# Optimization experiments

Measured on AMD Instinct MI355X. Metric: run time of the kernel, lower is better.

## Reference

```python
import math
import jax, jax.numpy as jnp
import numpy as np

D_MODEL = 1024
NUM_HEADS = 16
HEAD_DIM = D_MODEL // NUM_HEADS
B, T = 2, 2048


def setup_inputs() -> dict:
    key = jax.random.key(0)
    ks = jax.random.split(key, 11)
    s = 0.02
    inp = {
        'x':  jax.random.normal(ks[0], (B, T, D_MODEL), dtype=jnp.float32),
        'Wq': jax.random.normal(ks[1], (D_MODEL, D_MODEL), dtype=jnp.float32) * s,
        'bq': jax.random.normal(ks[2], (D_MODEL,), dtype=jnp.float32) * s,
        'Wk': jax.random.normal(ks[3], (D_MODEL, D_MODEL), dtype=jnp.float32) * s,
        'bk': jax.random.normal(ks[4], (D_MODEL,), dtype=jnp.float32) * s,
        'Wv': jax.random.normal(ks[5], (D_MODEL, D_MODEL), dtype=jnp.float32) * s,
        'bv': jax.random.normal(ks[6], (D_MODEL,), dtype=jnp.float32) * s,
        'Wt': jax.random.normal(ks[7], (D_MODEL, D_MODEL), dtype=jnp.float32) * s,
        'bt': jax.random.normal(ks[8], (D_MODEL,), dtype=jnp.float32) * s,
        'Wo': jax.random.normal(ks[9], (D_MODEL, D_MODEL), dtype=jnp.float32) * s,
        'bo': jax.random.normal(ks[10], (D_MODEL,), dtype=jnp.float32) * s,
    }
    return inp


def reference(x, Wq, bq, Wk, bk, Wv, bv, Wt, bt, Wo, bo):
    Bx, Tx, D = x.shape
    H, hd = NUM_HEADS, HEAD_DIM
    scale = 1.0 / math.sqrt(hd)

    def proj(W, b):
        # (B,T,D) -> (B,H,T,hd); torch Linear uses x @ W.T + b
        return (x @ W.T + b).reshape(Bx, Tx, H, hd).transpose(0, 2, 1, 3)

    q = proj(Wq, bq)
    k = proj(Wk, bk)
    v = proj(Wv, bv)
    t = proj(Wt, bt)

    # dot-product term: (B,H,T,T)
    scores = jnp.einsum('bhqd,bhkd->bhqk', q, k)
    # triplet term: cumsum over key positions of (k*v)/sqrt(hd)
    kv_cumsum = jnp.cumsum(k * v * scale, axis=2)  # (B,H,T,hd)
    scores = scores + jnp.einsum('bhqd,bhkd->bhqk', q * t, kv_cumsum)
    scores = scores * scale

    # causal mask: position j > i forbidden
    causal = jnp.tril(jnp.ones((Tx, Tx), dtype=bool))
    scores = jnp.where(causal[None, None], scores, jnp.float32(-jnp.inf))

    attn = jax.nn.softmax(scores, axis=-1)  # stable max-subtract internally
    out = jnp.einsum('bhqk,bhkd->bhqd', attn, v)
    out = out.transpose(0, 2, 1, 3).reshape(Bx, Tx, D)
    return out @ Wo.T + bo
```

## Files before the change

kernel.cpp:

```cpp
#include <hip/hip_runtime.h>
#include <hip/hip_bf16.h>

typedef unsigned short u16;
typedef __attribute__((ext_vector_type(8))) short bf16x8;
typedef __attribute__((ext_vector_type(4))) float f32x4;
typedef __attribute__((ext_vector_type(4))) unsigned int u32x4;

#define LOG2E 1.44269504088896340736f

static __device__ __forceinline__ float b2f(u16 u) {
    union { float f; unsigned int i; } v; v.i = ((unsigned int)u) << 16; return v.f;
}
static __device__ __forceinline__ u16 f2b(float f) {
    unsigned int x = __builtin_bit_cast(unsigned int, f);
    unsigned int r = (x + 0x7fffu + ((x >> 16) & 1u)) >> 16;
    return (u16)r;
}
static __device__ __forceinline__ void gll16(const u16* g, u16* l) {
    __builtin_amdgcn_global_load_lds((const __attribute__((address_space(1))) void*)g,
                                     (__attribute__((address_space(3))) void*)l, 16, 0, 0);
}
static __device__ __forceinline__ float fexp2(float x) {
    float r; asm("v_exp_f32 %0, %1" : "=v"(r) : "v"(x)); return r;
}

__global__ __launch_bounds__(256) void cvt_all(const float* __restrict__ x,
                                               const float* __restrict__ w0, const float* __restrict__ w1,
                                               const float* __restrict__ w2, const float* __restrict__ w3,
                                               const float* __restrict__ w4, u16* __restrict__ dst) {
    size_t c = (size_t)blockIdx.x * 256 + threadIdx.x;
    size_t e = c * 4;
    const float* s; size_t off;
    const size_t M4 = (size_t)4 << 20, M1 = (size_t)1 << 20;
    if (e < M4) { s = x; off = e; }
    else {
        size_t r = e - M4; int wsel = (int)(r >> 20); off = r & (M1 - 1);
        s = wsel == 0 ? w0 : wsel == 1 ? w1 : wsel == 2 ? w2 : wsel == 3 ? w3 : w4;
    }
    float4 v = *(const float4*)(s + off);
    u16* d = dst + e;
    d[0] = f2b(v.x); d[1] = f2b(v.y); d[2] = f2b(v.z); d[3] = f2b(v.w);
}

template<int WM>
static __device__ __forceinline__ void gemm_body(const u16* __restrict__ A, const u16* __restrict__ W,
                                                 const float* __restrict__ bias, void* __restrict__ outp,
                                                 int mode, u16* Al, u16* Bl, int tm, int tn) {
    const int tid = threadIdx.x, lane = tid & 63, w = tid >> 6;
    const int wr = w >> 1, wc = w & 1;
    const int l15 = lane & 15, lhi = lane >> 4;

    f32x4 acc[WM][4] = {};

    for (int kt = 0; kt < 16; ++kt) {
        const int k0 = kt * 64;
        #pragma unroll
        for (int i = 0; i < WM; ++i) {
            int rl = i * 32 + w * 8 + (lane >> 3);
            int c  = (lane & 7) ^ (rl & 7);
            gll16(A + (size_t)(tm + rl) * 1024 + k0 + c * 8, Al + (i * 32 + w * 8) * 64);
        }
        #pragma unroll
        for (int i = 0; i < 4; ++i) {
            int rl = i * 32 + w * 8 + (lane >> 3);
            int c  = (lane & 7) ^ (rl & 7);
            gll16(W + (size_t)(tn + rl) * 1024 + k0 + c * 8, Bl + (i * 32 + w * 8) * 64);
        }
        __syncthreads();
        #pragma unroll
        for (int ks = 0; ks < 2; ++ks) {
            bf16x8 af[WM], bfr[4];
            #pragma unroll
            for (int mi = 0; mi < WM; ++mi) {
                int row = wr * (WM * 16) + mi * 16 + l15;
                int cc = (ks * 4 + lhi) ^ (row & 7);
                af[mi] = *(const bf16x8*)(Al + row * 64 + cc * 8);
            }
            #pragma unroll
            for (int ni = 0; ni < 4; ++ni) {
                int row = wc * 64 + ni * 16 + l15;
                int cc = (ks * 4 + lhi) ^ (row & 7);
                bfr[ni] = *(const bf16x8*)(Bl + row * 64 + cc * 8);
            }
            #pragma unroll
            for (int mi = 0; mi < WM; ++mi)
                #pragma unroll
                for (int ni = 0; ni < 4; ++ni)
                    acc[mi][ni] = __builtin_amdgcn_mfma_f32_16x16x32_bf16(af[mi], bfr[ni], acc[mi][ni], 0, 0, 0);
        }
        __syncthreads();
    }

    float bcol[4];
    #pragma unroll
    for (int ni = 0; ni < 4; ++ni) bcol[ni] = bias[tn + wc * 64 + ni * 16 + l15];

    #pragma unroll
    for (int mi = 0; mi < WM; ++mi)
        #pragma unroll
        for (int ni = 0; ni < 4; ++ni)
            #pragma unroll
            for (int r = 0; r < 4; ++r) {
                int rg = tm + wr * (WM * 16) + mi * 16 + lhi * 4 + r;
                int cg = tn + wc * 64 + ni * 16 + l15;
                float v = acc[mi][ni][r] + bcol[ni];
                if (mode == 2) {
                    ((float*)outp)[(size_t)rg * 1024 + cg] = v;
                } else {
                    int b = rg >> 11, t = rg & 2047, h = cg >> 6, d = cg & 63;
                    if (mode == 0)
                        ((u16*)outp)[(((size_t)(b * 16 + h)) * 2048 + t) * 128 + d] = f2b(v);
                    else
                        ((u16*)outp)[(((size_t)(b * 16 + h)) * 2048 + t) * 64 + d] = f2b(v);
                }
            }
}

struct ProjArgs {
    const u16* W[4];
    const float* b[4];
    u16* out[4];
};

__global__ __launch_bounds__(256) void gemm_proj(const u16* __restrict__ A, ProjArgs pa) {
    __shared__ u16 Al[128 * 64];
    __shared__ u16 Bl[128 * 64];
    const int d = blockIdx.x + 8 * blockIdx.y + 256 * blockIdx.z;
    const int c = d & 7, wtn = d >> 3;
    const int z = c >> 1, yh = c & 1;
    const int yy = yh * 16 + (wtn >> 3);
    const int xx = wtn & 7;
    gemm_body<4>(A, pa.W[z], pa.b[z], pa.out[z], (z < 2) ? 0 : 1, Al, Bl, yy * 128, xx * 128);
}


__global__ __launch_bounds__(256) void gemm_out2(const u16* __restrict__ A, const u16* __restrict__ W,
                                                 const float* __restrict__ bias, void* __restrict__ out) {
    __shared__ u16 Al[64 * 64];
    __shared__ u16 Bl[128 * 64];
    const int d = blockIdx.x + 8 * blockIdx.y;
    const int c = d & 7, wtn = d >> 3;
    const int yy = c * 8 + (wtn >> 3);
    const int xx = wtn & 7;
    gemm_body<2>(A, W, bias, out, 2, Al, Bl, yy * 64, xx * 128);
}

__global__ __launch_bounds__(256) void fuse_small(u16* __restrict__ Qa, const u16* __restrict__ Tp,
                                                  const u16* __restrict__ V, u16* __restrict__ VT,
                                                  u16* __restrict__ Ka) {
    __shared__ char shmem[64 * 72 * 2];
    const int b = blockIdx.x, tid = threadIdx.x;

    if (b < 2048) {
        int idx = b * 256 + tid;
        int tg = idx >> 3, dc = idx & 7;
        bf16x8 q = *(const bf16x8*)(Qa + (size_t)tg * 128 + dc * 8);
        bf16x8 tt = *(const bf16x8*)(Tp + (size_t)tg * 64 + dc * 8);
        bf16x8 o;
        #pragma unroll
        for (int j = 0; j < 8; ++j) o[j] = (short)f2b(b2f((u16)q[j]) * b2f((u16)tt[j]));
        *(bf16x8*)(Qa + (size_t)tg * 128 + 64 + dc * 8) = o;
    } else if (b < 3072) {
        u16 (*tile)[72] = (u16(*)[72])shmem;
        const int r0 = b - 2048;
        const int bh = r0 >> 5, tc = r0 & 31;
        const u16* Vh = V + ((size_t)bh * 2048 + tc * 64) * 64;
        u16* VTh = VT + (size_t)bh * 64 * 2048 + tc * 64;
        for (int i = 0; i < 2; ++i) {
            int f = i * 256 + tid;
            int r = f >> 3, dc = f & 7;
            bf16x8 v = *(const bf16x8*)(Vh + r * 64 + dc * 8);
            #pragma unroll
            for (int j = 0; j < 8; ++j) tile[dc * 8 + j][r] = (u16)v[j];
        }
        __syncthreads();
        for (int i = 0; i < 2; ++i) {
            int f = i * 256 + tid;
            int d = f >> 3, t8 = (f & 7) * 8;
            bf16x8 o;
            #pragma unroll
            for (int j = 0; j < 8; ++j) {
                int pos = t8 + j;
                int key = (pos & 32) + 16 * ((pos >> 2) & 1) + 4 * ((pos >> 3) & 3) + (pos & 3);
                o[j] = (short)tile[d][key];
            }
            *(bf16x8*)(VTh + (size_t)d * 2048 + t8) = o;
        }
    } else {
        float4* sums = (float4*)shmem;
        const int r0 = b - 3072;
        const int bh = r0 & 31, dg = r0 >> 5;
        u16* Kh = Ka + (size_t)bh * 2048 * 128;
        const u16* Vh = V + (size_t)bh * 2048 * 64;
        const int quad = tid & 3, c = tid >> 2;
        const int d0 = dg * 16 + quad * 4;
        float s0 = 0.f, s1 = 0.f, s2 = 0.f, s3 = 0.f;
        for (int i = 0; i < 32; ++i) {
            int t = c * 32 + i;
            ushort4 kv = *(const ushort4*)(Kh + (size_t)t * 128 + d0);
            ushort4 vv = *(const ushort4*)(Vh + (size_t)t * 64 + d0);
            s0 += b2f(kv.x) * b2f(vv.x);
            s1 += b2f(kv.y) * b2f(vv.y);
            s2 += b2f(kv.z) * b2f(vv.z);
            s3 += b2f(kv.w) * b2f(vv.w);
        }
        float4 sv; sv.x = s0; sv.y = s1; sv.z = s2; sv.w = s3;
        sums[c * 4 + quad] = sv;
        __syncthreads();
        float4 run; run.x = run.y = run.z = run.w = 0.f;
        for (int cc = 0; cc < c; ++cc) {
            float4 ss = sums[cc * 4 + quad];
            run.x += ss.x; run.y += ss.y; run.z += ss.z; run.w += ss.w;
        }
        for (int i = 0; i < 32; ++i) {
            int t = c * 32 + i;
            ushort4 kv = *(const ushort4*)(Kh + (size_t)t * 128 + d0);
            ushort4 vv = *(const ushort4*)(Vh + (size_t)t * 64 + d0);
            run.x += b2f(kv.x) * b2f(vv.x);
            run.y += b2f(kv.y) * b2f(vv.y);
            run.z += b2f(kv.z) * b2f(vv.z);
            run.w += b2f(kv.w) * b2f(vv.w);
            ushort4 o;
            o.x = f2b(run.x * 0.125f); o.y = f2b(run.y * 0.125f);
            o.z = f2b(run.z * 0.125f); o.w = f2b(run.w * 0.125f);
            *(ushort4*)(Kh + (size_t)t * 128 + 64 + d0) = o;
        }
    }
}

__global__ __launch_bounds__(256, 3) void attn5(const u16* __restrict__ Qa, const u16* __restrict__ Ka,
                                                const u16* __restrict__ VT, u16* __restrict__ Obuf) {
    const int wg = blockIdx.x;
    const int xcd = wg & 7, slot = wg >> 3;
    const int bh = xcd * 4 + (slot >> 4);
    const int qp = slot & 15;
    const int tiL = qp, tiH = 31 - qp;
    const int q0L = tiL * 64, q0H = tiH * 64;
    const int NT = tiH + 1;
    const u16* Qh = Qa + (size_t)bh * 2048 * 128;
    const u16* Kh = Ka + (size_t)bh * 2048 * 128;
    const u16* VTh = VT + (size_t)bh * 64 * 2048;

    __shared__ u16 Kl[2][64 * 128];
    __shared__ u16 Vl[2][64 * 64];

    const int tid = threadIdx.x, lane = tid & 63, w = tid >> 6;
    const int l15 = lane & 15, lhi = lane >> 4;
    const float SC = 0.125f * LOG2E;

    bf16x8 qfL[4], qfH[4];
    #pragma unroll
    for (int ks = 0; ks < 4; ++ks) {
        bf16x8 a = *(const bf16x8*)(Qh + (size_t)(q0L + w * 16 + l15) * 128 + ks * 32 + lhi * 8);
        bf16x8 b = *(const bf16x8*)(Qh + (size_t)(q0H + w * 16 + l15) * 128 + ks * 32 + lhi * 8);
        bf16x8 oa, ob;
        #pragma unroll
        for (int j = 0; j < 8; ++j) {
            oa[j] = (short)f2b(b2f((u16)a[j]) * SC);
            ob[j] = (short)f2b(b2f((u16)b[j]) * SC);
        }
        qfL[ks] = oa; qfH[ks] = ob;
    }

    f32x4 accL[4] = {}, accH[4] = {};
    float lsL = 0.f, lsH = 0.f;

    auto STAGE = [&](int buf, int ti) {
        const int kv0 = ti * 64;
        #pragma unroll
        for (int i = 0; i < 4; ++i) {
            int lr = i * 16 + w * 4 + lhi;
            int c = l15 ^ (lr & 15);
            gll16(Kh + (size_t)(kv0 + lr) * 128 + c * 8, &Kl[buf][(i * 16 + w * 4) * 128]);
        }
        #pragma unroll
        for (int i = 0; i < 2; ++i) {
            int dr = i * 32 + w * 8 + (lane >> 3);
            int c = (lane & 7) ^ (dr & 7);
            gll16(VTh + (size_t)dr * 2048 + kv0 + c * 8, &Vl[buf][(i * 32 + w * 8) * 64]);
        }
    };

    STAGE(0, 0);
    asm volatile("s_waitcnt vmcnt(0)" ::: "memory");
    __builtin_amdgcn_s_barrier();

    for (int ti = 0; ti < NT; ++ti) {
        const int cur = ti & 1;
        if (ti + 1 < NT) STAGE(cur ^ 1, ti + 1);
        const bool doL = (ti <= tiL);

        f32x4 sH[4] = {}, sL[4] = {};
        #pragma unroll
        for (int ks = 0; ks < 4; ++ks) {
            bf16x8 kf[4];
            #pragma unroll
            for (int k2 = 0; k2 < 4; ++k2) {
                int kl = k2 * 16 + l15;
                int cc = (ks * 4 + lhi) ^ l15;
                kf[k2] = *(const bf16x8*)(&Kl[cur][kl * 128 + cc * 8]);
            }
            __builtin_amdgcn_s_setprio(1);
            #pragma unroll
            for (int k2 = 0; k2 < 4; ++k2)
                sH[k2] = __builtin_amdgcn_mfma_f32_16x16x32_bf16(kf[k2], qfH[ks], sH[k2], 0, 0, 0);
            if (doL) {
                #pragma unroll
                for (int k2 = 0; k2 < 4; ++k2)
                    sL[k2] = __builtin_amdgcn_mfma_f32_16x16x32_bf16(kf[k2], qfL[ks], sL[k2], 0, 0, 0);
            }
            __builtin_amdgcn_s_setprio(0);
        }

        auto FINISH = [&](f32x4* sacc, f32x4* acc, float& lsum, bool diag) {
            float p[4][4];
            #pragma unroll
            for (int k2 = 0; k2 < 4; ++k2)
                #pragma unroll
                for (int r = 0; r < 4; ++r) {
                    float s = sacc[k2][r];
                    if (diag) {
                        int key = k2 * 16 + lhi * 4 + r;
                        int qq = w * 16 + l15;
                        s = (key <= qq) ? s : -1e30f;
                    }
                    float pe = fexp2(s);
                    p[k2][r] = pe;
                    lsum += pe;
                }
            bf16x8 pf[2];
            #pragma unroll
            for (int ks2 = 0; ks2 < 2; ++ks2) {
                unsigned int w0, w1, w2, w3;
                asm("v_cvt_pk_bf16_f32 %0, %1, %2" : "=v"(w0) : "v"(p[2 * ks2][0]),     "v"(p[2 * ks2][1]));
                asm("v_cvt_pk_bf16_f32 %0, %1, %2" : "=v"(w1) : "v"(p[2 * ks2][2]),     "v"(p[2 * ks2][3]));
                asm("v_cvt_pk_bf16_f32 %0, %1, %2" : "=v"(w2) : "v"(p[2 * ks2 + 1][0]), "v"(p[2 * ks2 + 1][1]));
                asm("v_cvt_pk_bf16_f32 %0, %1, %2" : "=v"(w3) : "v"(p[2 * ks2 + 1][2]), "v"(p[2 * ks2 + 1][3]));
                u32x4 t = {w0, w1, w2, w3};
                pf[ks2] = __builtin_bit_cast(bf16x8, t);
            }
            #pragma unroll
            for (int ks2 = 0; ks2 < 2; ++ks2) {
                __builtin_amdgcn_s_setprio(1);
                #pragma unroll
                for (int dt = 0; dt < 4; ++dt) {
                    int dd = dt * 16 + l15;
                    int cc = (ks2 * 4 + lhi) ^ (dd & 7);
                    bf16x8 vf = *(const bf16x8*)(&Vl[cur][dd * 64 + cc * 8]);
                    acc[dt] = __builtin_amdgcn_mfma_f32_16x16x32_bf16(pf[ks2], vf, acc[dt], 0, 0, 0);
                }
                __builtin_amdgcn_s_setprio(0);
            }
        };

        FINISH(sH, accH, lsH, ti == tiH);
        if (doL) FINISH(sL, accL, lsL, ti == tiL);

        asm volatile("s_waitcnt vmcnt(0)" ::: "memory");
        __builtin_amdgcn_s_barrier();
    }

    lsH += __shfl_xor(lsH, 16, 64); lsH += __shfl_xor(lsH, 32, 64);
    lsL += __shfl_xor(lsL, 16, 64); lsL += __shfl_xor(lsL, 32, 64);
    float invH[4], invL[4];
    #pragma unroll
    for (int r = 0; r < 4; ++r) {
        invH[r] = 1.0f / __shfl(lsH, lhi * 4 + r, 64);
        invL[r] = 1.0f / __shfl(lsL, lhi * 4 + r, 64);
    }
    #pragma unroll
    for (int dt = 0; dt < 4; ++dt)
        #pragma unroll
        for (int r = 0; r < 4; ++r) {
            int cr = lhi * 4 + r;
            int dd = dt * 16 + l15;
            int qgL = q0L + w * 16 + cr;
            int qgH = q0H + w * 16 + cr;
            size_t nL = (size_t)(bh >> 4) * 2048 + qgL;
            size_t nH = (size_t)(bh >> 4) * 2048 + qgH;
            Obuf[nL * 1024 + (bh & 15) * 64 + dd] = f2b(accL[dt][r] * invL[r]);
            Obuf[nH * 1024 + (bh & 15) * 64 + dd] = f2b(accH[dt][r] * invH[r]);
        }
}

extern "C" void kernel_launch(void* const* d_in, const int* in_sizes, int n_in,
                              void* d_out, int out_size, void* d_ws, size_t ws_size,
                              hipStream_t stream) {
    (void)in_sizes; (void)n_in; (void)out_size; (void)ws_size;
    const float* x  = (const float*)d_in[0];
    const float* Wq = (const float*)d_in[1];
    const float* bq = (const float*)d_in[2];
    const float* Wk = (const float*)d_in[3];
    const float* bk = (const float*)d_in[4];
    const float* Wv = (const float*)d_in[5];
    const float* bv = (const float*)d_in[6];
    const float* Wt = (const float*)d_in[7];
    const float* bt = (const float*)d_in[8];
    const float* Wo = (const float*)d_in[9];
    const float* bo = (const float*)d_in[10];

    const size_t M1 = 1024u * 1024u;
    u16* xb   = (u16*)d_ws;
    u16* wq   = xb + 4 * M1;
    u16* wk   = wq + M1;
    u16* wv   = wk + M1;
    u16* wt   = wv + M1;
    u16* wo   = wt + M1;
    u16* Qa   = wo + M1;
    u16* Kaa  = Qa + 8 * M1;
    u16* Vtm  = Kaa + 8 * M1;
    u16* Ttm  = Vtm + 4 * M1;
    u16* Obuf = Ttm + 4 * M1;
    u16* VTg  = xb;

    cvt_all<<<9216, 256, 0, stream>>>(x, Wq, Wk, Wv, Wt, Wo, xb);

    ProjArgs pa;
    pa.W[0] = wq; pa.W[1] = wk; pa.W[2] = wv; pa.W[3] = wt;
    pa.b[0] = bq; pa.b[1] = bk; pa.b[2] = bv; pa.b[3] = bt;
    pa.out[0] = Qa; pa.out[1] = Kaa; pa.out[2] = Vtm; pa.out[3] = Ttm;
    gemm_proj<<<dim3(8, 32, 4), 256, 0, stream>>>(xb, pa);

    fuse_small<<<3200, 256, 0, stream>>>(Qa, Ttm, Vtm, VTg, Kaa);

    attn5<<<512, 256, 0, stream>>>(Qa, Kaa, VTg, Obuf);

    gemm_out2<<<dim3(8, 64), 256, 0, stream>>>(Obuf, wo, bo, d_out);
}
```

Measured before the change: 138.6 us.

## Triple-buffer K/V tiles and software-pipeline QK of next tile with softmax-PV

The attention kernel moves from double to triple buffering of K and V tiles in LDS, with separate staging so that K is prefetched three tiles ahead and V two tiles ahead. The loop is software-pipelined: the QK^T MFMAs for tile ti+1 are issued before the exp/PV work for tile ti, so matrix and vector work can overlap. Partial vmcnt waits replace the full drain. In exchange, LDS use rises to three buffers and launch bounds drop from 3 to 2 blocks per CU, and holding two sets of score accumulators adds register pressure.

Result: no change. 140.2 us (+1.1%).

```diff
diff --git a/kernel.cpp b/kernel.cpp
--- a/kernel.cpp
+++ b/kernel.cpp
@@ -132,7 +132,6 @@
     const int xx = wtn & 7;
     gemm_body<4>(A, pa.W[z], pa.b[z], pa.out[z], (z < 2) ? 0 : 1, Al, Bl, yy * 128, xx * 128);
 }
-
 
 __global__ __launch_bounds__(256) void gemm_out2(const u16* __restrict__ A, const u16* __restrict__ W,
                                                  const float* __restrict__ bias, void* __restrict__ out) {
@@ -228,7 +227,7 @@
     }
 }
 
-__global__ __launch_bounds__(256, 3) void attn5(const u16* __restrict__ Qa, const u16* __restrict__ Ka,
+__global__ __launch_bounds__(256, 2) void attn8(const u16* __restrict__ Qa, const u16* __restrict__ Ka,
                                                 const u16* __restrict__ VT, u16* __restrict__ Obuf) {
     const int wg = blockIdx.x;
     const int xcd = wg & 7, slot = wg >> 3;
@@ -241,8 +240,8 @@
     const u16* Kh = Ka + (size_t)bh * 2048 * 128;
     const u16* VTh = VT + (size_t)bh * 64 * 2048;
 
-    __shared__ u16 Kl[2][64 * 128];
-    __shared__ u16 Vl[2][64 * 64];
+    __shared__ u16 Kl[3][64 * 128];
+    __shared__ u16 Vl[3][64 * 64];
 
     const int tid = threadIdx.x, lane = tid & 63, w = tid >> 6;
     const int l15 = lane & 15, lhi = lane >> 4;
@@ -265,32 +264,27 @@
     f32x4 accL[4] = {}, accH[4] = {};
     float lsL = 0.f, lsH = 0.f;
 
-    auto STAGE = [&](int buf, int ti) {
-        const int kv0 = ti * 64;
+    auto STAGE_V = [&](int ti) {
+        const int kv0 = ti * 64, buf = ti % 3;
+        #pragma unroll
+        for (int i = 0; i < 2; ++i) {
+            int dr = i * 32 + w * 8 + (lane >> 3);
+            int c = (lane & 7) ^ (dr & 7);
+            gll16(VTh + (size_t)dr * 2048 + kv0 + c * 8, &Vl[buf][(i * 32 + w * 8) * 64]);
+        }
+    };
+    auto STAGE_K = [&](int ti) {
+        const int kv0 = ti * 64, buf = ti % 3;
         #pragma unroll
         for (int i = 0; i < 4; ++i) {
             int lr = i * 16 + w * 4 + lhi;
             int c = l15 ^ (lr & 15);
             gll16(Kh + (size_t)(kv0 + lr) * 128 + c * 8, &Kl[buf][(i * 16 + w * 4) * 128]);
         }
-        #pragma unroll
-        for (int i = 0; i < 2; ++i) {
-            int dr = i * 32 + w * 8 + (lane >> 3);
-            int c = (lane & 7) ^ (dr & 7);
-            gll16(VTh + (size_t)dr * 2048 + kv0 + c * 8, &Vl[buf][(i * 32 + w * 8) * 64]);
-        }
     };
 
-    STAGE(0, 0);
-    asm volatile("s_waitcnt vmcnt(0)" ::: "memory");
-    __builtin_amdgcn_s_barrier();
-
-    for (int ti = 0; ti < NT; ++ti) {
-        const int cur = ti & 1;
-        if (ti + 1 < NT) STAGE(cur ^ 1, ti + 1);
-        const bool doL = (ti <= tiL);
-
-        f32x4 sH[4] = {}, sL[4] = {};
+    auto QK = [&](int ti, bool doL, f32x4* sH, f32x4* sL) {
+        const int cur = ti % 3;
         #pragma unroll
         for (int ks = 0; ks < 4; ++ks) {
             bf16x8 kf[4];
@@ -311,53 +305,77 @@
             }
             __builtin_amdgcn_s_setprio(0);
         }
-
-        auto FINISH = [&](f32x4* sacc, f32x4* acc, float& lsum, bool diag) {
-            float p[4][4];
-            #pragma unroll
-            for (int k2 = 0; k2 < 4; ++k2)
-                #pragma unroll
-                for (int r = 0; r < 4; ++r) {
-                    float s = sacc[k2][r];
-                    if (diag) {
-                        int key = k2 * 16 + lhi * 4 + r;
-                        int qq = w * 16 + l15;
-                        s = (key <= qq) ? s : -1e30f;
-                    }
-                    float pe = fexp2(s);
-                    p[k2][r] = pe;
-                    lsum += pe;
+    };
+
+    auto FINISH = [&](int ti, f32x4* sacc, f32x4* acc, float& lsum, bool diag) {
+        const int cur = ti % 3;
+        float p[4][4];
+        #pragma unroll
+        for (int k2 = 0; k2 < 4; ++k2)
+            #pragma unroll
+            for (int r = 0; r < 4; ++r) {
+                float s = sacc[k2][r];
+                if (diag) {
+                    int key = k2 * 16 + lhi * 4 + r;
+                    int qq = w * 16 + l15;
+                    s = (key <= qq) ? s : -1e30f;
                 }
-            bf16x8 pf[2];
-            #pragma unroll
-            for (int ks2 = 0; ks2 < 2; ++ks2) {
-                unsigned int w0, w1, w2, w3;
-                asm("v_cvt_pk_bf16_f32 %0, %1, %2" : "=v"(w0) : "v"(p[2 * ks2][0]),     "v"(p[2 * ks2][1]));
-                asm("v_cvt_pk_bf16_f32 %0, %1, %2" : "=v"(w1) : "v"(p[2 * ks2][2]),     "v"(p[2 * ks2][3]));
-                asm("v_cvt_pk_bf16_f32 %0, %1, %2" : "=v"(w2) : "v"(p[2 * ks2 + 1][0]), "v"(p[2 * ks2 + 1][1]));
-                asm("v_cvt_pk_bf16_f32 %0, %1, %2" : "=v"(w3) : "v"(p[2 * ks2 + 1][2]), "v"(p[2 * ks2 + 1][3]));
-                u32x4 t = {w0, w1, w2, w3};
-                pf[ks2] = __builtin_bit_cast(bf16x8, t);
-            }
-            #pragma unroll
-            for (int ks2 = 0; ks2 < 2; ++ks2) {
-                __builtin_amdgcn_s_setprio(1);
-                #pragma unroll
-                for (int dt = 0; dt < 4; ++dt) {
-                    int dd = dt * 16 + l15;
-                    int cc = (ks2 * 4 + lhi) ^ (dd & 7);
-                    bf16x8 vf = *(const bf16x8*)(&Vl[cur][dd * 64 + cc * 8]);
-                    acc[dt] = __builtin_amdgcn_mfma_f32_16x16x32_bf16(pf[ks2], vf, acc[dt], 0, 0, 0);
-                }
-                __builtin_amdgcn_s_setprio(0);
-            }
-        };
-
-        FINISH(sH, accH, lsH, ti == tiH);
-        if (doL) FINISH(sL, accL, lsL, ti == tiL);
-
-        asm volatile("s_waitcnt vmcnt(0)" ::: "memory");
-        __builtin_amdgcn_s_barrier();
+                float pe = fexp2(s);
+                p[k2][r] = pe;
+                lsum += pe;
+            }
+        bf16x8 pf[2];
+        #pragma unroll
+        for (int ks2 = 0; ks2 < 2; ++ks2) {
+            unsigned int w0, w1, w2, w3;
+            asm("v_cvt_pk_bf16_f32 %0, %1, %2" : "=v"(w0) : "v"(p[2 * ks2][0]),     "v"(p[2 * ks2][1]));
+            asm("v_cvt_pk_bf16_f32 %0, %1, %2" : "=v"(w1) : "v"(p[2 * ks2][2]),     "v"(p[2 * ks2][3]));
+            asm("v_cvt_pk_bf16_f32 %0, %1, %2" : "=v"(w2) : "v"(p[2 * ks2 + 1][0]), "v"(p[2 * ks2 + 1][1]));
+            asm("v_cvt_pk_bf16_f32 %0, %1, %2" : "=v"(w3) : "v"(p[2 * ks2 + 1][2]), "v"(p[2 * ks2 + 1][3]));
+            u32x4 t = {w0, w1, w2, w3};
+            pf[ks2] = __builtin_bit_cast(bf16x8, t);
+        }
+        #pragma unroll
+        for (int ks2 = 0; ks2 < 2; ++ks2) {
+            __builtin_amdgcn_s_setprio(1);
+            #pragma unroll
+            for (int dt = 0; dt < 4; ++dt) {
+                int dd = dt * 16 + l15;
+                int cc = (ks2 * 4 + lhi) ^ (dd & 7);
+                bf16x8 vf = *(const bf16x8*)(&Vl[cur][dd * 64 + cc * 8]);
+                acc[dt] = __builtin_amdgcn_mfma_f32_16x16x32_bf16(pf[ks2], vf, acc[dt], 0, 0, 0);
+            }
+            __builtin_amdgcn_s_setprio(0);
+        }
+    };
+
+    STAGE_V(0); STAGE_V(1);
+    STAGE_K(0); STAGE_K(1); STAGE_K(2);
+    asm volatile("s_waitcnt vmcnt(0)" ::: "memory");
+    __builtin_amdgcn_s_barrier();
+
+    f32x4 sHc[4] = {}, sLc[4] = {};
+    QK(0, true, sHc, sLc);
+
+    for (int ti = 0; ti < NT; ++ti) {
+        if (ti + 2 < NT) STAGE_V(ti + 2);
+        if (ti + 3 < NT) STAGE_K(ti + 3);
+
+        f32x4 sHn[4] = {}, sLn[4] = {};
+        const bool doLn = (ti + 1 <= tiL);
+        if (ti + 1 < NT) QK(ti + 1, doLn, sHn, sLn);
+
+        FINISH(ti, sHc, accH, lsH, ti == tiH);
+        if (ti <= tiL) FINISH(ti, sLc, accL, lsL, ti == tiL);
+
+        #pragma unroll
+        for (int k2 = 0; k2 < 4; ++k2) { sHc[k2] = sHn[k2]; sLc[k2] = sLn[k2]; }
+
+        if (ti + 1 < NT) {
+            if (ti + 3 < NT) asm volatile("s_waitcnt vmcnt(4)" ::: "memory");
+            else             asm volatile("s_waitcnt vmcnt(0)" ::: "memory");
+            __builtin_amdgcn_s_barrier();
+        }
     }
 
     lsH += __shfl_xor(lsH, 16, 64); lsH += __shfl_xor(lsH, 32, 64);
@@ -423,7 +441,7 @@
 
     fuse_small<<<3200, 256, 0, stream>>>(Qa, Ttm, Vtm, VTg, Kaa);
 
-    attn5<<<512, 256, 0, stream>>>(Qa, Kaa, VTg, Obuf);
+    attn8<<<512, 256, 0, stream>>>(Qa, Kaa, VTg, Obuf);
 
     gemm_out2<<<dim3(8, 64), 256, 0, stream>>>(Obuf, wo, bo, d_out);
 }
```

## Split paired-query attention blocks into one query tile per workgroup

Applied to the files above, without the earlier changes.

The attention kernel no longer pairs a low and a high query tile in one workgroup to balance causal work. It now launches 1024 workgroups, each handling a single 64-row query tile, with the longest tiles scheduled first. This halves register use per workgroup and drops the occupancy hint, aiming for more resident waves and simpler code. The cost is that K/V tiles are no longer shared between two query tiles, so staging traffic per unit of compute rises, and load balance now depends on the descending-order schedule.

Result: no change. 140.9 us (+1.6%).

```diff
diff --git a/kernel.cpp b/kernel.cpp
--- a/kernel.cpp
+++ b/kernel.cpp
@@ -132,7 +132,6 @@
     const int xx = wtn & 7;
     gemm_body<4>(A, pa.W[z], pa.b[z], pa.out[z], (z < 2) ? 0 : 1, Al, Bl, yy * 128, xx * 128);
 }
-
 
 __global__ __launch_bounds__(256) void gemm_out2(const u16* __restrict__ A, const u16* __restrict__ W,
                                                  const float* __restrict__ bias, void* __restrict__ out) {
@@ -228,15 +227,14 @@
     }
 }
 
-__global__ __launch_bounds__(256, 3) void attn5(const u16* __restrict__ Qa, const u16* __restrict__ Ka,
-                                                const u16* __restrict__ VT, u16* __restrict__ Obuf) {
+__global__ __launch_bounds__(256) void attn9(const u16* __restrict__ Qa, const u16* __restrict__ Ka,
+                                             const u16* __restrict__ VT, u16* __restrict__ Obuf) {
     const int wg = blockIdx.x;
     const int xcd = wg & 7, slot = wg >> 3;
-    const int bh = xcd * 4 + (slot >> 4);
-    const int qp = slot & 15;
-    const int tiL = qp, tiH = 31 - qp;
-    const int q0L = tiL * 64, q0H = tiH * 64;
-    const int NT = tiH + 1;
+    const int bh = xcd * 4 + (slot >> 5);
+    const int qb = 31 - (slot & 31);
+    const int q0 = qb * 64;
+    const int NT = qb + 1;
     const u16* Qh = Qa + (size_t)bh * 2048 * 128;
     const u16* Kh = Ka + (size_t)bh * 2048 * 128;
     const u16* VTh = VT + (size_t)bh * 64 * 2048;
@@ -248,22 +246,18 @@
     const int l15 = lane & 15, lhi = lane >> 4;
     const float SC = 0.125f * LOG2E;
 
-    bf16x8 qfL[4], qfH[4];
+    bf16x8 qf[4];
     #pragma unroll
     for (int ks = 0; ks < 4; ++ks) {
-        bf16x8 a = *(const bf16x8*)(Qh + (size_t)(q0L + w * 16 + l15) * 128 + ks * 32 + lhi * 8);
-        bf16x8 b = *(const bf16x8*)(Qh + (size_t)(q0H + w * 16 + l15) * 128 + ks * 32 + lhi * 8);
-        bf16x8 oa, ob;
-        #pragma unroll
-        for (int j = 0; j < 8; ++j) {
-            oa[j] = (short)f2b(b2f((u16)a[j]) * SC);
-            ob[j] = (short)f2b(b2f((u16)b[j]) * SC);
-        }
-        qfL[ks] = oa; qfH[ks] = ob;
+        bf16x8 a = *(const bf16x8*)(Qh + (size_t)(q0 + w * 16 + l15) * 128 + ks * 32 + lhi * 8);
+        bf16x8 oa;
+        #pragma unroll
+        for (int j = 0; j < 8; ++j) oa[j] = (short)f2b(b2f((u16)a[j]) * SC);
+        qf[ks] = oa;
     }
 
-    f32x4 accL[4] = {}, accH[4] = {};
-    float lsL = 0.f, lsH = 0.f;
+    f32x4 acc[4] = {};
+    float lsum = 0.f;
 
     auto STAGE = [&](int buf, int ti) {
         const int kv0 = ti * 64;
@@ -288,9 +282,8 @@
     for (int ti = 0; ti < NT; ++ti) {
         const int cur = ti & 1;
         if (ti + 1 < NT) STAGE(cur ^ 1, ti + 1);
-        const bool doL = (ti <= tiL);
-
-        f32x4 sH[4] = {}, sL[4] = {};
+
+        f32x4 s4[4] = {};
         #pragma unroll
         for (int ks = 0; ks < 4; ++ks) {
             bf16x8 kf[4];
@@ -303,83 +296,67 @@
             __builtin_amdgcn_s_setprio(1);
             #pragma unroll
             for (int k2 = 0; k2 < 4; ++k2)
-                sH[k2] = __builtin_amdgcn_mfma_f32_16x16x32_bf16(kf[k2], qfH[ks], sH[k2], 0, 0, 0);
-            if (doL) {
-                #pragma unroll
-                for (int k2 = 0; k2 < 4; ++k2)
-                    sL[k2] = __builtin_amdgcn_mfma_f32_16x16x32_bf16(kf[k2], qfL[ks], sL[k2], 0, 0, 0);
-            }
+                s4[k2] = __builtin_amdgcn_mfma_f32_16x16x32_bf16(kf[k2], qf[ks], s4[k2], 0, 0, 0);
             __builtin_amdgcn_s_setprio(0);
         }
 
-        auto FINISH = [&](f32x4* sacc, f32x4* acc, float& lsum, bool diag) {
-            float p[4][4];
-            #pragma unroll
-            for (int k2 = 0; k2 < 4; ++k2)
-                #pragma unroll
-                for (int r = 0; r < 4; ++r) {
-                    float s = sacc[k2][r];
-                    if (diag) {
-                        int key = k2 * 16 + lhi * 4 + r;
-                        int qq = w * 16 + l15;
-                        s = (key <= qq) ? s : -1e30f;
-                    }
-                    float pe = fexp2(s);
-                    p[k2][r] = pe;
-                    lsum += pe;
+        const bool diag = (ti == NT - 1);
+        float p[4][4];
+        #pragma unroll
+        for (int k2 = 0; k2 < 4; ++k2)
+            #pragma unroll
+            for (int r = 0; r < 4; ++r) {
+                float s = s4[k2][r];
+                if (diag) {
+                    int key = k2 * 16 + lhi * 4 + r;
+                    int qq = w * 16 + l15;
+                    s = (key <= qq) ? s : -1e30f;
                 }
-            bf16x8 pf[2];
-            #pragma unroll
-            for (int ks2 = 0; ks2 < 2; ++ks2) {
-                unsigned int w0, w1, w2, w3;
-                asm("v_cvt_pk_bf16_f32 %0, %1, %2" : "=v"(w0) : "v"(p[2 * ks2][0]),     "v"(p[2 * ks2][1]));
-                asm("v_cvt_pk_bf16_f32 %0, %1, %2" : "=v"(w1) : "v"(p[2 * ks2][2]),     "v"(p[2 * ks2][3]));
-                asm("v_cvt_pk_bf16_f32 %0, %1, %2" : "=v"(w2) : "v"(p[2 * ks2 + 1][0]), "v"(p[2 * ks2 + 1][1]));
-                asm("v_cvt_pk_bf16_f32 %0, %1, %2" : "=v"(w3) : "v"(p[2 * ks2 + 1][2]), "v"(p[2 * ks2 + 1][3]));
-                u32x4 t = {w0, w1, w2, w3};
-                pf[ks2] = __builtin_bit_cast(bf16x8, t);
-            }
-            #pragma unroll
-            for (int ks2 = 0; ks2 < 2; ++ks2) {
-                __builtin_amdgcn_s_setprio(1);
-                #pragma unroll
-                for (int dt = 0; dt < 4; ++dt) {
-                    int dd = dt * 16 + l15;
-                    int cc = (ks2 * 4 + lhi) ^ (dd & 7);
-                    bf16x8 vf = *(const bf16x8*)(&Vl[cur][dd * 64 + cc * 8]);
-                    acc[dt] = __builtin_amdgcn_mfma_f32_16x16x32_bf16(pf[ks2], vf, acc[dt], 0, 0, 0);
-                }
-                __builtin_amdgcn_s_setprio(0);
-            }
-        };
-
-        FINISH(sH, accH, lsH, ti == tiH);
-        if (doL) FINISH(sL, accL, lsL, ti == tiL);
+                float pe = fexp2(s);
+                p[k2][r] = pe;
+                lsum += pe;
+            }
+        bf16x8 pf[2];
+        #pragma unroll
+        for (int ks2 = 0; ks2 < 2; ++ks2) {
+            unsigned int w0, w1, w2, w3;
+            asm("v_cvt_pk_bf16_f32 %0, %1, %2" : "=v"(w0) : "v"(p[2 * ks2][0]),     "v"(p[2 * ks2][1]));
+            asm("v_cvt_pk_bf16_f32 %0, %1, %2" : "=v"(w1) : "v"(p[2 * ks2][2]),     "v"(p[2 * ks2][3]));
+            asm("v_cvt_pk_bf16_f32 %0, %1, %2" : "=v"(w2) : "v"(p[2 * ks2 + 1][0]), "v"(p[2 * ks2 + 1][1]));
+            asm("v_cvt_pk_bf16_f32 %0, %1, %2" : "=v"(w3) : "v"(p[2 * ks2 + 1][2]), "v"(p[2 * ks2 + 1][3]));
+            u32x4 t = {w0, w1, w2, w3};
+            pf[ks2] = __builtin_bit_cast(bf16x8, t);
+        }
+        #pragma unroll
+        for (int ks2 = 0; ks2 < 2; ++ks2) {
+            __builtin_amdgcn_s_setprio(1);
+            #pragma unroll
+            for (int dt = 0; dt < 4; ++dt) {
+                int dd = dt * 16 + l15;
+                int cc = (ks2 * 4 + lhi) ^ (dd & 7);
+                bf16x8 vf = *(const bf16x8*)(&Vl[cur][dd * 64 + cc * 8]);
+                acc[dt] = __builtin_amdgcn_mfma_f32_16x16x32_bf16(pf[ks2], vf, acc[dt], 0, 0, 0);
+            }
+            __builtin_amdgcn_s_setprio(0);
+        }
 
         asm volatile("s_waitcnt vmcnt(0)" ::: "memory");
         __builtin_amdgcn_s_barrier();
     }
 
-    lsH += __shfl_xor(lsH, 16, 64); lsH += __shfl_xor(lsH, 32, 64);
-    lsL += __shfl_xor(lsL, 16, 64); lsL += __shfl_xor(lsL, 32, 64);
-    float invH[4], invL[4];
+    lsum += __shfl_xor(lsum, 16, 64); lsum += __shfl_xor(lsum, 32, 64);
+    float inv[4];
     #pragma unroll
-    for (int r = 0; r < 4; ++r) {
-        invH[r] = 1.0f / __shfl(lsH, lhi * 4 + r, 64);
-        invL[r] = 1.0f / __shfl(lsL, lhi * 4 + r, 64);
-    }
+    for (int r = 0; r < 4; ++r) inv[r] = 1.0f / __shfl(lsum, lhi * 4 + r, 64);
     #pragma unroll
     for (int dt = 0; dt < 4; ++dt)
         #pragma unroll
         for (int r = 0; r < 4; ++r) {
             int cr = lhi * 4 + r;
             int dd = dt * 16 + l15;
-            int qgL = q0L + w * 16 + cr;
-            int qgH = q0H + w * 16 + cr;
-            size_t nL = (size_t)(bh >> 4) * 2048 + qgL;
-            size_t nH = (size_t)(bh >> 4) * 2048 + qgH;
-            Obuf[nL * 1024 + (bh & 15) * 64 + dd] = f2b(accL[dt][r] * invL[r]);
-            Obuf[nH * 1024 + (bh & 15) * 64 + dd] = f2b(accH[dt][r] * invH[r]);
+            int qg = q0 + w * 16 + cr;
+            size_t n = (size_t)(bh >> 4) * 2048 + qg;
+            Obuf[n * 1024 + (bh & 15) * 64 + dd] = f2b(acc[dt][r] * inv[r]);
         }
 }
 
@@ -423,7 +400,7 @@
 
     fuse_small<<<3200, 256, 0, stream>>>(Qa, Ttm, Vtm, VTg, Kaa);
 
-    attn5<<<512, 256, 0, stream>>>(Qa, Kaa, VTg, Obuf);
+    attn9<<<1024, 256, 0, stream>>>(Qa, Kaa, VTg, Obuf);
 
     gemm_out2<<<dim3(8, 64), 256, 0, stream>>>(Obuf, wo, bo, d_out);
 }
```
